# Kernel tuning notes

Hardware: AMD Instinct MI355X
Metric: run time of the kernel (lower is better)

## Reference

```python
import jax, jax.numpy as jnp
import numpy as np

D_MODEL = 768
NUM_HEADS = 12
D_K = D_MODEL // NUM_HEADS
D_FF = 3072
EPS = 1e-5


def _layer_norm(x, gamma, beta):
    mu = jnp.mean(x, axis=-1, keepdims=True)
    var = jnp.mean(jnp.square(x - mu), axis=-1, keepdims=True)
    return (x - mu) * jax.lax.rsqrt(var + EPS) * gamma + beta


def setup_inputs() -> dict:
    key = jax.random.key(0)
    ks = jax.random.split(key, 16)
    s = 1.0 / np.sqrt(D_MODEL)
    sf = 1.0 / np.sqrt(D_FF)
    inp = {
        "x": jax.random.normal(ks[0], (2, 2048, D_MODEL), dtype=jnp.float32),
        "Wq": jax.random.uniform(ks[1], (D_MODEL, D_MODEL), jnp.float32, -s, s),
        "bq": jax.random.uniform(ks[2], (D_MODEL,), jnp.float32, -s, s),
        "Wk": jax.random.uniform(ks[3], (D_MODEL, D_MODEL), jnp.float32, -s, s),
        "bk": jax.random.uniform(ks[4], (D_MODEL,), jnp.float32, -s, s),
        "Wv": jax.random.uniform(ks[5], (D_MODEL, D_MODEL), jnp.float32, -s, s),
        "bv": jax.random.uniform(ks[6], (D_MODEL,), jnp.float32, -s, s),
        "Wo": jax.random.uniform(ks[7], (D_MODEL, D_MODEL), jnp.float32, -s, s),
        "bo": jax.random.uniform(ks[8], (D_MODEL,), jnp.float32, -s, s),
        "W1": jax.random.uniform(ks[9], (D_MODEL, D_FF), jnp.float32, -s, s),
        "b1": jax.random.uniform(ks[10], (D_FF,), jnp.float32, -s, s),
        "W2": jax.random.uniform(ks[11], (D_FF, D_MODEL), jnp.float32, -sf, sf),
        "b2": jax.random.uniform(ks[12], (D_MODEL,), jnp.float32, -sf, sf),
        "g1": jnp.ones((D_MODEL,), jnp.float32),
        "be1": jnp.zeros((D_MODEL,), jnp.float32),
        "g2": jnp.ones((D_MODEL,), jnp.float32),
        "be2": jnp.zeros((D_MODEL,), jnp.float32),
    }
    return inp


def reference(x, Wq, bq, Wk, bk, Wv, bv, Wo, bo, W1, b1, W2, b2, g1, be1, g2, be2):
    B, S, _ = x.shape

    def split(h):  # (B,S,D) -> (B,H,S,Dk)
        return h.reshape(B, S, NUM_HEADS, D_K).transpose(0, 2, 1, 3)

    q = split(x @ Wq + bq)
    k = split(x @ Wk + bk)
    v = split(x @ Wv + bv)

    # naive attention: materialize full (B,H,S,S) scores as in the original
    scores = jnp.einsum("bhsd,bhtd->bhst", q, k) / np.sqrt(D_K)
    attn = jax.nn.softmax(scores, axis=-1)
    ctx = jnp.einsum("bhst,bhtd->bhsd", attn, v)
    ctx = ctx.transpose(0, 2, 1, 3).reshape(B, S, D_MODEL)
    attn_out = ctx @ Wo + bo

    x = _layer_norm(x + attn_out, g1, be1)
    ff = jax.nn.relu(x @ W1 + b1) @ W2 + b2
    x = _layer_norm(x + ff, g2, be2)
    return x
```

## Files before the change

### kernel.cpp

```cpp
#include <hip/hip_runtime.h>
#include <cstdint>


typedef unsigned short u16;
typedef unsigned int u32;
typedef __attribute__((ext_vector_type(4))) float f32x4;
typedef __attribute__((ext_vector_type(8))) short s16x8;
typedef __attribute__((ext_vector_type(4))) u16  u16x4;
typedef __attribute__((ext_vector_type(2))) u32  u32x2;

#define AS1 __attribute__((address_space(1)))
#define AS3 __attribute__((address_space(3)))

__device__ __forceinline__ u16 f2b(float f) {
  union { float f; unsigned u; } v; v.f = f;
  unsigned r = v.u + 0x7FFFu + ((v.u >> 16) & 1u);
  return (u16)(r >> 16);
}

__device__ __forceinline__ void gl_lds16(const void* g, void* lds_uniform_base) {
  __builtin_amdgcn_global_load_lds((const AS1 void*)g, (AS3 void*)lds_uniform_base, 16, 0, 0);
}

__device__ __forceinline__ f32x4 mfma16(s16x8 a, s16x8 b, f32x4 c) {
  return __builtin_amdgcn_mfma_f32_16x16x32_bf16(a, b, c, 0, 0, 0);
}

__device__ __forceinline__ u32 cvt_pk_bf16(float lo, float hi) {
  u32 r;
  asm("v_cvt_pk_bf16_f32 %0, %1, %2" : "=v"(r) : "v"(lo), "v"(hi));
  return r;
}

__global__ __launch_bounds__(256) void prep(
    const float* __restrict__ Wq, const float* __restrict__ Wk,
    const float* __restrict__ Wv, const float* __restrict__ Wo,
    const float* __restrict__ W1, const float* __restrict__ W2,
    const float* __restrict__ bq, const float* __restrict__ bk,
    const float* __restrict__ bv, const float* __restrict__ x,
    u16* __restrict__ Wqkv_t, u16* __restrict__ Wo_t,
    u16* __restrict__ W1_t, u16* __restrict__ W2_t,
    float* __restrict__ bqkv, u16* __restrict__ Xb, int convBlocks) {
  __shared__ float ts[32][33];
  const int bid = blockIdx.x;
  const int tx = threadIdx.x, ty = threadIdx.y;
  if (bid < 6912) {
    const float* W; u16* Wt; int K, N, tile;
    if (bid < 2304) {
      int w = bid / 576; tile = bid - w * 576; K = 768; N = 768;
      W = (w == 0) ? Wq : (w == 1) ? Wk : (w == 2) ? Wv : Wo;
      Wt = (w < 3) ? Wqkv_t + (size_t)w * 768 * 768 : Wo_t;
    } else if (bid < 4608) {
      tile = bid - 2304; K = 768; N = 3072; W = W1; Wt = W1_t;
    } else {
      tile = bid - 4608; K = 3072; N = 768; W = W2; Wt = W2_t;
    }
    int ntx = N >> 5;
    int n0 = (tile % ntx) * 32, k0 = (tile / ntx) * 32;
#pragma unroll
    for (int yy = 0; yy < 32; yy += 8)
      ts[ty + yy][tx] = W[(size_t)(k0 + ty + yy) * N + n0 + tx];
    __syncthreads();
#pragma unroll
    for (int yy = 0; yy < 32; yy += 8)
      Wt[(size_t)(n0 + ty + yy) * K + k0 + tx] = f2b(ts[tx][ty + yy]);
  } else if (bid < 6912 + convBlocks) {
    int t = ty * 32 + tx;
    size_t i = ((size_t)(bid - 6912) * 256 + t) * 4;
    f32x4 v = *(const f32x4*)(x + i);
    u16x4 o;
#pragma unroll
    for (int k = 0; k < 4; ++k) o[k] = f2b(v[k]);
    *(u16x4*)(Xb + i) = o;
  } else {
    int t = ty * 32 + tx;
    int i = (bid - 6912 - convBlocks) * 256 + t;
    if (i < 2304) bqkv[i] = (i < 768) ? bq[i] : (i < 1536) ? bk[i - 768] : bv[i - 1536];
  }
}

__global__ __launch_bounds__(256) void transpose_v(const u16* __restrict__ Vh,
                                                   u16* __restrict__ Vt) {
  __shared__ u16 tile[32][33];
  int bh = blockIdx.z;
  int d0 = blockIdx.x * 32, s0 = blockIdx.y * 32;
  const u16* src = Vh + (size_t)bh * 2048 * 64;
  u16* dst = Vt + (size_t)bh * 64 * 2048;
  int x = threadIdx.x, y = threadIdx.y;
#pragma unroll
  for (int yy = 0; yy < 32; yy += 8)
    tile[y + yy][x] = src[(size_t)(s0 + y + yy) * 64 + d0 + x];
  __syncthreads();
#pragma unroll
  for (int yy = 0; yy < 32; yy += 8)
    dst[(size_t)(d0 + y + yy) * 2048 + s0 + x] = tile[x][y + yy];
}

template <int MODE>
__global__ __launch_bounds__(256) void gemm_bt(const u16* __restrict__ A,
                                               const u16* __restrict__ Bt,
                                               const float* __restrict__ bias,
                                               float* __restrict__ Cf, u16* __restrict__ Cb,
                                               u16* __restrict__ Qo, u16* __restrict__ Ko,
                                               u16* __restrict__ Vo, int M, int N, int K,
                                               int Klen) {
  __shared__ __align__(16) u16 lsA[128 * 64];
  __shared__ __align__(16) u16 lsB[128 * 64];
  const int tid = threadIdx.x;
  const int lane = tid & 63, wave = tid >> 6;
  const int lr = lane & 15, lh = lane >> 4;
  const int wr = wave >> 1, wc = wave & 1;

  int bx, by, bz;
  {
    int nx = gridDim.x, ny = gridDim.y, nz = gridDim.z;
    int total = nx * ny * nz;
    int lin = blockIdx.x + nx * (blockIdx.y + ny * blockIdx.z);
    if ((total & 7) == 0) {
      int key = (lin & 7) * (total >> 3) + (lin >> 3);
      by = key % ny;
      int t2 = key / ny;
      bz = t2 % nz;
      bx = t2 / nz;
    } else {
      bx = blockIdx.x; by = blockIdx.y; bz = blockIdx.z;
    }
  }
  const int m0 = by * 128;
  const int n0 = bx * 128;
  const int kB = bz * Klen;

  f32x4 acc[4][4];
#pragma unroll
  for (int i = 0; i < 4; ++i)
#pragma unroll
    for (int j = 0; j < 4; ++j) acc[i][j] = f32x4{0.f, 0.f, 0.f, 0.f};

  const size_t aBase = (size_t)m0 * K;
  const size_t bBase = (size_t)n0 * K;
  const int srow8 = tid >> 3;
  const int scolE = (((tid & 7) * 16) ^ ((srow8 & 7) << 4)) >> 1;
  const int xk = (lr & 7) << 4;

  for (int kt = kB; kt < kB + Klen; kt += 64) {
#pragma unroll
    for (int i = 0; i < 4; ++i) {
      int row = i * 32 + srow8;
      int ldsOff = i * 4096 + wave * 1024;
      gl_lds16(A + aBase + (size_t)row * K + kt + scolE, (char*)lsA + ldsOff);
      gl_lds16(Bt + bBase + (size_t)row * K + kt + scolE, (char*)lsB + ldsOff);
    }
    __syncthreads();
    const char* baA = (const char*)lsA;
    const char* baB = (const char*)lsB;
#pragma unroll
    for (int ks = 0; ks < 2; ++ks) {
      int cb = (ks * 64 + lh * 16) ^ xk;
      s16x8 a[4], b[4];
#pragma unroll
      for (int i = 0; i < 4; ++i) {
        a[i] = *(const s16x8*)(baA + (wr * 64 + i * 16 + lr) * 128 + cb);
        b[i] = *(const s16x8*)(baB + (wc * 64 + i * 16 + lr) * 128 + cb);
      }
#pragma unroll
      for (int i = 0; i < 4; ++i)
#pragma unroll
        for (int j = 0; j < 4; ++j) acc[i][j] = mfma16(a[i], b[j], acc[i][j]);
    }
    __syncthreads();
  }

  float* CfP = Cf + (size_t)bz * M * N;
#pragma unroll
  for (int i = 0; i < 4; ++i) {
    int growb = m0 + wr * 64 + i * 16 + lh * 4;
#pragma unroll
    for (int j = 0; j < 4; ++j) {
      int col = n0 + wc * 64 + j * 16 + lr;
      float bv = (MODE != 0 || bz == 0) ? bias[col] : 0.f;
#pragma unroll
      for (int q = 0; q < 4; ++q) {
        int grow = growb + q;
        float v = acc[i][j][q] + bv;
        if (MODE == 0) {
          CfP[(size_t)grow * N + col] = v;
        } else if (MODE == 1) {
          Cb[(size_t)grow * N + col] = f2b(fmaxf(v, 0.f));
        } else {
          int sel = col / 768;
          int c2 = col - sel * 768;
          int h = c2 >> 6, d = c2 & 63;
          int b = grow >> 11, s = grow & 2047;
          size_t idx = (((size_t)(b * 12 + h)) * 2048 + s) * 64 + d;
          float vv = (sel == 0) ? v * 0.1803368801f : v;
          u16* dst = (sel == 0) ? Qo : (sel == 1) ? Ko : Vo;
          dst[idx] = f2b(vv);
        }
      }
    }
  }
}

__global__ __launch_bounds__(512) void attn(const u16* __restrict__ Qh,
                                            const u16* __restrict__ Kh,
                                            const u16* __restrict__ Vt,
                                            float* __restrict__ Op,
                                            float* __restrict__ ml,
                                            int nbh, int ntile) {
  __shared__ __align__(16) u16 lsK[2][64 * 64];
  __shared__ __align__(16) u16 lsV[2][64 * 64];
  __shared__ __align__(16) u16 lsP[8][16 * 64];
  const int tid = threadIdx.x, lane = tid & 63, wave = tid >> 6;
  const int lr = lane & 15, lh = lane >> 4;

  int bx = blockIdx.x, bh = blockIdx.y, z = blockIdx.z;
  {
    int nz = gridDim.z;
    int total = 16 * nbh * nz;
    if ((total & 7) == 0) {
      int lin = bx + 16 * (bh + nbh * z);
      int nl = (lin & 7) * (total >> 3) + (lin >> 3);
      bx = nl & 15;
      bh = (nl >> 4) % nbh;
      z = nl / (16 * nbh);
    }
  }
  const int q0 = bx * 128 + wave * 16;
  const size_t kvBase = (size_t)bh * 2048 * 64;
  const int tB = z * ntile;

  const int srow = tid >> 3;
  const int scol = (((tid & 7) * 16) ^ ((srow & 7) << 4)) >> 1;
  const u16* kSrcBase = Kh + kvBase + (size_t)srow * 64 + scol;
  const u16* vSrcBase = Vt + kvBase + (size_t)srow * 2048 + scol;

  s16x8 qf[2];
#pragma unroll
  for (int ks = 0; ks < 2; ++ks)
    qf[ks] = *(const s16x8*)(Qh + kvBase + (size_t)(q0 + lr) * 64 + ks * 32 + lh * 8);

  f32x4 oacc[4];
  float mrow = -1e30f, lsum = 0.f;
#pragma unroll
  for (int d = 0; d < 4; ++d) oacc[d] = f32x4{0.f, 0.f, 0.f, 0.f};

  gl_lds16(kSrcBase + (size_t)tB * 4096, (char*)lsK[0] + wave * 1024);
  gl_lds16(vSrcBase + tB * 64,           (char*)lsV[0] + wave * 1024);

  for (int it = 0; it < ntile; ++it) {
    const int cur = it & 1;
    __syncthreads();

    s16x8 kb[2][4];
#pragma unroll
    for (int ks = 0; ks < 2; ++ks)
#pragma unroll
      for (int j = 0; j < 4; ++j) {
        int r = j * 16 + lr;
        kb[ks][j] = *(const s16x8*)((const char*)lsK[cur] + r * 128 +
                                    ((ks * 64 + lh * 16) ^ ((r & 7) << 4)));
      }

    if (it + 1 < ntile) {
      int t = tB + it + 1;
      gl_lds16(kSrcBase + (size_t)t * 4096, (char*)lsK[cur ^ 1] + wave * 1024);
      gl_lds16(vSrcBase + t * 64,           (char*)lsV[cur ^ 1] + wave * 1024);
    }

    f32x4 st[4];
#pragma unroll
    for (int j = 0; j < 4; ++j) st[j] = f32x4{0.f, 0.f, 0.f, 0.f};
    __builtin_amdgcn_s_setprio(1);
#pragma unroll
    for (int ks = 0; ks < 2; ++ks)
#pragma unroll
      for (int j = 0; j < 4; ++j) st[j] = mfma16(kb[ks][j], qf[ks], st[j]);
    __builtin_amdgcn_s_setprio(0);

    float mx;
    {
      float a0 = fmaxf(fmaxf(st[0][0], st[0][1]), fmaxf(st[0][2], st[0][3]));
      float a1 = fmaxf(fmaxf(st[1][0], st[1][1]), fmaxf(st[1][2], st[1][3]));
      float a2 = fmaxf(fmaxf(st[2][0], st[2][1]), fmaxf(st[2][2], st[2][3]));
      float a3 = fmaxf(fmaxf(st[3][0], st[3][1]), fmaxf(st[3][2], st[3][3]));
      mx = fmaxf(fmaxf(a0, a1), fmaxf(a2, a3));
      mx = fmaxf(mx, __shfl_xor(mx, 16));
      mx = fmaxf(mx, __shfl_xor(mx, 32));
    }
    if (__any(mx > mrow + 11.f)) {
      float mn = fmaxf(mrow, mx);
      float al = exp2f(mrow - mn);
      mrow = mn;
      lsum *= al;
#pragma unroll
      for (int d = 0; d < 4; ++d)
#pragma unroll
        for (int q = 0; q < 4; ++q) oacc[d][q] *= al;
    }

    float ps = 0.f;
#pragma unroll
    for (int j = 0; j < 4; ++j) {
      float p0 = exp2f(st[j][0] - mrow);
      float p1 = exp2f(st[j][1] - mrow);
      float p2 = exp2f(st[j][2] - mrow);
      float p3 = exp2f(st[j][3] - mrow);
      ps += (p0 + p1) + (p2 + p3);
      u32x2 pk;
      pk.x = cvt_pk_bf16(p0, p1);
      pk.y = cvt_pk_bf16(p2, p3);
      *(u32x2*)((char*)lsP[wave] + lr * 128 + ((j * 32 + lh * 8) ^ ((lr & 7) << 4))) = pk;
    }
    ps += __shfl_xor(ps, 16);
    ps += __shfl_xor(ps, 32);
    lsum += ps;

    __builtin_amdgcn_s_setprio(1);
#pragma unroll
    for (int ks = 0; ks < 2; ++ks) {
      s16x8 pa = *(const s16x8*)((const char*)lsP[wave] + lr * 128 +
                                 ((ks * 64 + lh * 16) ^ ((lr & 7) << 4)));
#pragma unroll
      for (int d = 0; d < 4; ++d) {
        int r = d * 16 + lr;
        s16x8 vb = *(const s16x8*)((const char*)lsV[cur] + r * 128 +
                                   ((ks * 64 + lh * 16) ^ ((r & 7) << 4)));
        oacc[d] = mfma16(vb, pa, oacc[d]);
      }
    }
    __builtin_amdgcn_s_setprio(0);
  }

  {
    int s = q0 + lr;
    size_t r = ((size_t)z * nbh + bh) * 2048 + s;
#pragma unroll
    for (int d = 0; d < 4; ++d)
      *(f32x4*)(Op + r * 64 + d * 16 + lh * 4) = oacc[d];
    if (lh == 0) { ml[r * 2] = mrow; ml[r * 2 + 1] = lsum; }
  }
}

template <int NZ>
__global__ __launch_bounds__(256) void attn_combine(const float* __restrict__ Op,
                                                    const float* __restrict__ ml,
                                                    u16* __restrict__ ctx, int nbh) {
  size_t i = (size_t)blockIdx.x * 256 + threadIdx.x;
  int d4 = (int)(i & 15);
  size_t rs = i >> 4;
  size_t zs = (size_t)nbh * 2048;
  float m[NZ], l[NZ];
  float mx = -1e30f;
#pragma unroll
  for (int p = 0; p < NZ; ++p) {
    m[p] = ml[(p * zs + rs) * 2];
    l[p] = ml[(p * zs + rs) * 2 + 1];
    mx = fmaxf(mx, m[p]);
  }
  float wsum = 0.f, a[NZ];
#pragma unroll
  for (int p = 0; p < NZ; ++p) { a[p] = exp2f(m[p] - mx); wsum += l[p] * a[p]; }
  float inv = 1.f / wsum;
  f32x4 o = f32x4{0.f, 0.f, 0.f, 0.f};
#pragma unroll
  for (int p = 0; p < NZ; ++p) {
    f32x4 op = *(const f32x4*)(Op + (p * zs + rs) * 64 + d4 * 4);
#pragma unroll
    for (int k = 0; k < 4; ++k) o[k] += op[k] * a[p];
  }
  int bh = (int)(rs >> 11), s = (int)(rs & 2047);
  int b = bh / 12, h = bh - b * 12;
  u16x4 r;
#pragma unroll
  for (int k = 0; k < 4; ++k) r[k] = f2b(o[k] * inv);
  *(u16x4*)(ctx + ((size_t)(b * 2048 + s)) * 768 + h * 64 + d4 * 4) = r;
}

template <int NP>
__global__ __launch_bounds__(256) void resid_ln(const float* __restrict__ xin,
                                                const float* __restrict__ yp,
                                                size_t pstride,
                                                const float* __restrict__ gamma,
                                                const float* __restrict__ beta,
                                                float* __restrict__ outf,
                                                u16* __restrict__ outb) {
  const int row = blockIdx.x, t = threadIdx.x;
  const size_t base = (size_t)row * 768;
  float v[3], s = 0.f, s2 = 0.f;
#pragma unroll
  for (int k = 0; k < 3; ++k) {
    int c = t + k * 256;
    float val = xin[base + c];
#pragma unroll
    for (int p = 0; p < NP; ++p) val += yp[p * pstride + base + c];
    v[k] = val; s += val; s2 += val * val;
  }
#pragma unroll
  for (int off = 32; off > 0; off >>= 1) {
    s += __shfl_down(s, off, 64);
    s2 += __shfl_down(s2, off, 64);
  }
  __shared__ float red[8];
  int lane = t & 63, wave = t >> 6;
  if (lane == 0) { red[wave] = s; red[4 + wave] = s2; }
  __syncthreads();
  s = red[0] + red[1] + red[2] + red[3];
  s2 = red[4] + red[5] + red[6] + red[7];
  const float inv = 1.f / 768.f;
  float mu = s * inv;
  float var = fmaxf(s2 * inv - mu * mu, 0.f);
  float rs = rsqrtf(var + 1e-5f);
#pragma unroll
  for (int k = 0; k < 3; ++k) {
    int c = t + k * 256;
    float o = (v[k] - mu) * rs * gamma[c] + beta[c];
    if (outf) outf[base + c] = o;
    if (outb) outb[base + c] = f2b(o);
  }
}

extern "C" void kernel_launch(void* const* d_in, const int* in_sizes, int n_in,
                              void* d_out, int out_size, void* d_ws, size_t ws_size,
                              hipStream_t stream) {
  const float* x   = (const float*)d_in[0];
  const float* Wq  = (const float*)d_in[1];
  const float* bq  = (const float*)d_in[2];
  const float* Wk  = (const float*)d_in[3];
  const float* bk  = (const float*)d_in[4];
  const float* Wv  = (const float*)d_in[5];
  const float* bv  = (const float*)d_in[6];
  const float* Wo  = (const float*)d_in[7];
  const float* bo  = (const float*)d_in[8];
  const float* W1  = (const float*)d_in[9];
  const float* b1  = (const float*)d_in[10];
  const float* W2  = (const float*)d_in[11];
  const float* b2  = (const float*)d_in[12];
  const float* g1  = (const float*)d_in[13];
  const float* be1 = (const float*)d_in[14];
  const float* g2  = (const float*)d_in[15];
  const float* be2 = (const float*)d_in[16];
  float* out = (float*)d_out;

  const int M = in_sizes[0] / 768;
  const int B = M / 2048;
  const int nbh = B * 12;

  char* ws = (char*)d_ws;
  size_t off = 0;
  auto alloc = [&](size_t bytes) -> void* {
    void* p = ws + off;
    off += (bytes + 255) & ~(size_t)255;
    return p;
  };
  u16*   Wqkv_t = (u16*)alloc((size_t)2304 * 768 * 2);
  u16*   Wo_t   = (u16*)alloc((size_t)768 * 768 * 2);
  u16*   W1_t   = (u16*)alloc((size_t)3072 * 768 * 2);
  u16*   W2_t   = (u16*)alloc((size_t)768 * 3072 * 2);
  float* bqkv   = (float*)alloc(2304 * 4);
  u16*   Xb     = (u16*)alloc((size_t)M * 768 * 2);
  u16*   Qh     = (u16*)alloc((size_t)M * 768 * 2);
  u16*   Kh     = (u16*)alloc((size_t)M * 768 * 2);
  u16*   Vh     = (u16*)alloc((size_t)M * 768 * 2);
  u16*   Vt     = (u16*)alloc((size_t)M * 768 * 2);

  size_t pstride = (size_t)M * 768;
  size_t fixedRest = pstride * 4  + pstride * 2  +
                     (size_t)M * 3072 * 2  + 4096;
  auto attnBytes = [&](int nz) {
    return (size_t)nz * nbh * 2048 * (64 + 2) * 4;
  };
  size_t reg4 = attnBytes(4) > pstride * 16 ? attnBytes(4) : pstride * 16;
  int ZSPLIT, FSPLIT;
  size_t regionBytes;
  if (off + reg4 + fixedRest <= ws_size) {
    ZSPLIT = 4; FSPLIT = 4; regionBytes = reg4;
  } else {
    ZSPLIT = 2; FSPLIT = 2;
    regionBytes = attnBytes(2) > pstride * 8 ? attnBytes(2) : pstride * 8;
  }
  float* region = (float*)alloc(regionBytes);
  float* Op   = region;
  float* ml   = region + (size_t)ZSPLIT * nbh * 2048 * 64;
  float* ffnPart  = region;
  float* projPart = (float*)Qh;
  float* x1f  = (float*)alloc(pstride * 4);
  u16*   x1b  = (u16*)alloc(pstride * 2);
  u16*   hb   = (u16*)alloc((size_t)M * 3072 * 2);
  u16*   ctx  = Xb;

  dim3 tb(32, 8);
  const int convBlocks = (M * 768) / 1024;
  prep<<<6912 + convBlocks + 9, tb, 0, stream>>>(
      Wq, Wk, Wv, Wo, W1, W2, bq, bk, bv, x,
      Wqkv_t, Wo_t, W1_t, W2_t, bqkv, Xb, convBlocks);

  gemm_bt<2><<<dim3(2304 / 128, M / 128), 256, 0, stream>>>(
      Xb, Wqkv_t, bqkv, nullptr, nullptr, Qh, Kh, Vh, M, 2304, 768, 768);

  transpose_v<<<dim3(2, 64, nbh), tb, 0, stream>>>(Vh, Vt);

  attn<<<dim3(16, nbh, ZSPLIT), 512, 0, stream>>>(Qh, Kh, Vt, Op, ml, nbh, 32 / ZSPLIT);
  if (ZSPLIT == 4)
    attn_combine<4><<<nbh * 128, 256, 0, stream>>>(Op, ml, ctx, nbh);
  else
    attn_combine<2><<<nbh * 128, 256, 0, stream>>>(Op, ml, ctx, nbh);

  gemm_bt<0><<<dim3(768 / 128, M / 128, 2), 256, 0, stream>>>(
      ctx, Wo_t, bo, projPart, nullptr, nullptr, nullptr, nullptr, M, 768, 768, 384);

  resid_ln<2><<<M, 256, 0, stream>>>(x, projPart, pstride, g1, be1, x1f, x1b);

  gemm_bt<1><<<dim3(3072 / 128, M / 128), 256, 0, stream>>>(
      x1b, W1_t, b1, nullptr, hb, nullptr, nullptr, nullptr, M, 3072, 768, 768);

  if (FSPLIT == 4) {
    gemm_bt<0><<<dim3(768 / 128, M / 128, 4), 256, 0, stream>>>(
        hb, W2_t, b2, ffnPart, nullptr, nullptr, nullptr, nullptr, M, 768, 3072, 768);
    resid_ln<4><<<M, 256, 0, stream>>>(x1f, ffnPart, pstride, g2, be2, out, nullptr);
  } else {
    gemm_bt<0><<<dim3(768 / 128, M / 128, 2), 256, 0, stream>>>(
        hb, W2_t, b2, ffnPart, nullptr, nullptr, nullptr, nullptr, M, 768, 3072, 1536);
    resid_ln<2><<<M, 256, 0, stream>>>(x1f, ffnPart, pstride, g2, be2, out, nullptr);
  }
}
```

Before: 222.9 us.

## Compute softmax row sums via MFMA with ones, use max3, fix attention split at 2

```diff
diff --git a/kernel.cpp b/kernel.cpp
--- a/kernel.cpp
+++ b/kernel.cpp
@@ -30,6 +30,10 @@
   u32 r;
   asm("v_cvt_pk_bf16_f32 %0, %1, %2" : "=v"(r) : "v"(lo), "v"(hi));
   return r;
+}
+
+__device__ __forceinline__ float max3f(float a, float b, float c) {
+  return fmaxf(fmaxf(a, b), c);
 }
 
 __global__ __launch_bounds__(256) void prep(
@@ -239,8 +243,13 @@
   for (int ks = 0; ks < 2; ++ks)
     qf[ks] = *(const s16x8*)(Qh + kvBase + (size_t)(q0 + lr) * 64 + ks * 32 + lh * 8);
 
+  s16x8 onesf;
+#pragma unroll
+  for (int k = 0; k < 8; ++k) onesf[k] = (short)0x3F80;
+
   f32x4 oacc[4];
-  float mrow = -1e30f, lsum = 0.f;
+  f32x4 aOnes = f32x4{0.f, 0.f, 0.f, 0.f};
+  float mrow = -1e30f;
 #pragma unroll
   for (int d = 0; d < 4; ++d) oacc[d] = f32x4{0.f, 0.f, 0.f, 0.f};
 
@@ -279,11 +288,12 @@
 
     float mx;
     {
-      float a0 = fmaxf(fmaxf(st[0][0], st[0][1]), fmaxf(st[0][2], st[0][3]));
-      float a1 = fmaxf(fmaxf(st[1][0], st[1][1]), fmaxf(st[1][2], st[1][3]));
-      float a2 = fmaxf(fmaxf(st[2][0], st[2][1]), fmaxf(st[2][2], st[2][3]));
-      float a3 = fmaxf(fmaxf(st[3][0], st[3][1]), fmaxf(st[3][2], st[3][3]));
-      mx = fmaxf(fmaxf(a0, a1), fmaxf(a2, a3));
+      float t0 = max3f(st[0][0], st[0][1], st[0][2]);
+      float t1 = max3f(st[0][3], st[1][0], st[1][1]);
+      float t2 = max3f(st[1][2], st[1][3], st[2][0]);
+      float t3 = max3f(st[2][1], st[2][2], st[2][3]);
+      float t4 = max3f(st[3][0], st[3][1], st[3][2]);
+      mx = fmaxf(max3f(t0, t1, t2), max3f(t3, t4, st[3][3]));
       mx = fmaxf(mx, __shfl_xor(mx, 16));
       mx = fmaxf(mx, __shfl_xor(mx, 32));
     }
@@ -291,35 +301,32 @@
       float mn = fmaxf(mrow, mx);
       float al = exp2f(mrow - mn);
       mrow = mn;
-      lsum *= al;
+#pragma unroll
+      for (int q = 0; q < 4; ++q) aOnes[q] *= al;
 #pragma unroll
       for (int d = 0; d < 4; ++d)
 #pragma unroll
         for (int q = 0; q < 4; ++q) oacc[d][q] *= al;
     }
 
-    float ps = 0.f;
 #pragma unroll
     for (int j = 0; j < 4; ++j) {
       float p0 = exp2f(st[j][0] - mrow);
       float p1 = exp2f(st[j][1] - mrow);
       float p2 = exp2f(st[j][2] - mrow);
       float p3 = exp2f(st[j][3] - mrow);
-      ps += (p0 + p1) + (p2 + p3);
       u32x2 pk;
       pk.x = cvt_pk_bf16(p0, p1);
       pk.y = cvt_pk_bf16(p2, p3);
       *(u32x2*)((char*)lsP[wave] + lr * 128 + ((j * 32 + lh * 8) ^ ((lr & 7) << 4))) = pk;
     }
-    ps += __shfl_xor(ps, 16);
-    ps += __shfl_xor(ps, 32);
-    lsum += ps;
 
     __builtin_amdgcn_s_setprio(1);
 #pragma unroll
     for (int ks = 0; ks < 2; ++ks) {
       s16x8 pa = *(const s16x8*)((const char*)lsP[wave] + lr * 128 +
                                  ((ks * 64 + lh * 16) ^ ((lr & 7) << 4)));
+      aOnes = mfma16(onesf, pa, aOnes);
 #pragma unroll
       for (int d = 0; d < 4; ++d) {
         int r = d * 16 + lr;
@@ -337,7 +344,7 @@
 #pragma unroll
     for (int d = 0; d < 4; ++d)
       *(f32x4*)(Op + r * 64 + d * 16 + lh * 4) = oacc[d];
-    if (lh == 0) { ml[r * 2] = mrow; ml[r * 2 + 1] = lsum; }
+    if (lh == 0) { ml[r * 2] = mrow; ml[r * 2 + 1] = aOnes[0]; }
   }
 }
 
@@ -466,17 +473,16 @@
   size_t pstride = (size_t)M * 768;
   size_t fixedRest = pstride * 4  + pstride * 2  +
                      (size_t)M * 3072 * 2  + 4096;
-  auto attnBytes = [&](int nz) {
-    return (size_t)nz * nbh * 2048 * (64 + 2) * 4;
-  };
-  size_t reg4 = attnBytes(4) > pstride * 16 ? attnBytes(4) : pstride * 16;
-  int ZSPLIT, FSPLIT;
+  const int ZSPLIT = 2;
+  size_t attnBytes = (size_t)ZSPLIT * nbh * 2048 * (64 + 2) * 4;
+  size_t reg4 = attnBytes > pstride * 16 ? attnBytes : pstride * 16;
+  int FSPLIT;
   size_t regionBytes;
   if (off + reg4 + fixedRest <= ws_size) {
-    ZSPLIT = 4; FSPLIT = 4; regionBytes = reg4;
+    FSPLIT = 4; regionBytes = reg4;
   } else {
-    ZSPLIT = 2; FSPLIT = 2;
-    regionBytes = attnBytes(2) > pstride * 8 ? attnBytes(2) : pstride * 8;
+    FSPLIT = 2;
+    regionBytes = attnBytes > pstride * 8 ? attnBytes : pstride * 8;
   }
   float* region = (float*)alloc(regionBytes);
   float* Op   = region;
@@ -500,10 +506,7 @@
   transpose_v<<<dim3(2, 64, nbh), tb, 0, stream>>>(Vh, Vt);
 
   attn<<<dim3(16, nbh, ZSPLIT), 512, 0, stream>>>(Qh, Kh, Vt, Op, ml, nbh, 32 / ZSPLIT);
-  if (ZSPLIT == 4)
-    attn_combine<4><<<nbh * 128, 256, 0, stream>>>(Op, ml, ctx, nbh);
-  else
-    attn_combine<2><<<nbh * 128, 256, 0, stream>>>(Op, ml, ctx, nbh);
+  attn_combine<2><<<nbh * 128, 256, 0, stream>>>(Op, ml, ctx, nbh);
 
   gemm_bt<0><<<dim3(768 / 128, M / 128, 2), 256, 0, stream>>>(
       ctx, Wo_t, bo, projPart, nullptr, nullptr, nullptr, nullptr, M, 768, 768, 384);
```

Result: faster. 215.7 us (-3.2%).
